# Kernel optimization log

Measured on AMD Instinct MI355X. Metric: run time of the kernel, lower is better.

Reference implementation:

```python
import jax, jax.numpy as jnp
import numpy as np

B, S, DIN, DOUT, A, T, H = 8, 1024, 1024, 1024, 4, 4, 8  # arity A, T cell types, hidden H


def setup_inputs() -> dict:
    key = jax.random.key(0)
    ks = jax.random.split(key, 6)
    x = jax.random.normal(ks[0], (B, S, DIN), jnp.float32)
    sc = 1.0 / np.sqrt(DIN).astype(np.float32)
    weight = jax.random.uniform(ks[1], (A * DOUT, DIN), jnp.float32, -sc, sc)
    bias = jax.random.uniform(ks[2], (A * DOUT,), jnp.float32, -sc, sc)
    # stacked per-cell-type MLP params: arity -> H -> 1 (tanh)
    cw1 = jax.random.normal(ks[3], (T, A, H), jnp.float32) / np.sqrt(A).astype(np.float32)
    cb1 = jnp.zeros((T, H), jnp.float32)
    cw2 = jax.random.normal(ks[4], (T, H), jnp.float32) / np.sqrt(H).astype(np.float32)
    cb2 = jnp.zeros((T,), jnp.float32)
    return {"x": x, "weight": weight, "bias": bias,
            "cw1": cw1, "cb1": cb1, "cw2": cw2, "cb2": cb2}


def reference(x, weight, bias, cw1, cb1, cw2, cb2):
    T_, A_, H_ = cw1.shape
    Dout = weight.shape[0] // A_
    G = Dout // T_  # neurons per cell type (cell_indices = contiguous blocks via np.repeat)
    # all_inputs = F.linear(input, weight, bias): (B, S, A*Dout)
    z = jnp.einsum('bsd,od->bso', x, weight) + bias
    # slice per-neuron arity chunks -> (B, S, T, G, A)
    z = z.reshape(z.shape[0], z.shape[1], T_, G, A_)
    # per-cell-type MLP applied to every neuron of that type (replaces Python loop)
    h = jnp.tanh(jnp.einsum('bstga,tah->bstgh', z, cw1) + cb1[:, None, :])
    o = jnp.einsum('bstgh,th->bstg', h, cw2) + cb2[:, None]
    # concat over neurons -> (B, S, Dout)
    return o.reshape(o.shape[0], o.shape[1], Dout)
```

## Files before the change

kernel.cpp:

```cpp
#include <hip/hip_runtime.h>


typedef __bf16 bf16x8 __attribute__((ext_vector_type(8)));
typedef float f32x4 __attribute__((ext_vector_type(4)));
typedef float f32x16 __attribute__((ext_vector_type(16)));

#define BM 256
#define BN 128
#define BK 64
#define KDIM 1024
#define A_ELEMS (BM * BK)
#define ZSTRIDE 132
#define XN8 (8192 * 1024 / 8)
#define WN8 (4096 * 1024 / 8)

__global__ __launch_bounds__(256) void cvt_bf16_kernel(
    const float* __restrict__ x, const float* __restrict__ w,
    __bf16* __restrict__ xb, __bf16* __restrict__ wb) {
    int i = blockIdx.x * 256 + threadIdx.x;
    const float* src;
    __bf16* dst;
    int j;
    if (i < XN8) { src = x; dst = xb; j = i; }
    else         { src = w; dst = wb; j = i - XN8; }
    const f32x4* p = (const f32x4*)src + 2 * (size_t)j;
    f32x4 a = p[0], b = p[1];
    bf16x8 o;
    o[0] = (__bf16)a[0]; o[1] = (__bf16)a[1]; o[2] = (__bf16)a[2]; o[3] = (__bf16)a[3];
    o[4] = (__bf16)b[0]; o[5] = (__bf16)b[1]; o[6] = (__bf16)b[2]; o[7] = (__bf16)b[3];
    ((bf16x8*)dst)[j] = o;
}

union __align__(16) SmemU {
    __bf16 stg[A_ELEMS + BN * BK];
    float  z[64 * ZSTRIDE];
};

__global__ __launch_bounds__(256, 2) void fused_gemm_mlp_kernel(
    const __bf16* __restrict__ Ag,
    const __bf16* __restrict__ Bg,
    const float* __restrict__ bias,
    const float* __restrict__ cw1,
    const float* __restrict__ cb1,
    const float* __restrict__ cw2,
    const float* __restrict__ cb2,
    float* __restrict__ out)
{
    __shared__ SmemU u;

    const int tid  = threadIdx.x;
    const int wave = tid >> 6;
    const int lane = tid & 63;
    const int wm = wave >> 1;
    const int wn = wave & 1;
    const int bn0 = blockIdx.x * BN;
    const int bm0 = blockIdx.y * BM;

    f32x16 acc[4][2] = {};

    const int srow  = lane >> 3;
    const int scol8 = (((lane & 7) ^ srow) * 8);

    const int lr5 = lane & 31;
    const int lk2 = lane >> 5;
    const int lx  = lane & 7;
    int a_base[4], b_base[4];
#pragma unroll
    for (int kh = 0; kh < 4; ++kh) {
        const int cx = ((kh * 2 + lk2) ^ lx) * 16;
        a_base[kh] = (wm * 128 + lr5) * (BK * 2) + cx;
        b_base[kh] = A_ELEMS * 2 + (wn * 64 + lr5) * (BK * 2) + cx;
    }
    const char* sb = (const char*)u.stg;

    for (int k0 = 0; k0 < KDIM; k0 += BK) {
#pragma unroll
        for (int c = 0; c < 8; ++c) {
            const int chunk = wave + c * 4;
            const __bf16* ga = Ag + (size_t)(bm0 + chunk * 8 + srow) * KDIM + k0 + scol8;
            __builtin_amdgcn_global_load_lds(
                (__attribute__((address_space(1))) void*)ga,
                (__attribute__((address_space(3))) void*)&u.stg[chunk * 8 * BK],
                16, 0, 0);
        }
#pragma unroll
        for (int c = 0; c < 4; ++c) {
            const int chunk = wave + c * 4;
            const __bf16* gb = Bg + (size_t)(bn0 + chunk * 8 + srow) * KDIM + k0 + scol8;
            __builtin_amdgcn_global_load_lds(
                (__attribute__((address_space(1))) void*)gb,
                (__attribute__((address_space(3))) void*)&u.stg[A_ELEMS + chunk * 8 * BK],
                16, 0, 0);
        }
        __syncthreads();

#pragma unroll
        for (int kh = 0; kh < 4; ++kh) {
            bf16x8 af[4], bfr[2];
#pragma unroll
            for (int mi = 0; mi < 4; ++mi)
                af[mi] = *(const bf16x8*)(sb + a_base[kh] + mi * 4096);
#pragma unroll
            for (int ni = 0; ni < 2; ++ni)
                bfr[ni] = *(const bf16x8*)(sb + b_base[kh] + ni * 4096);
#pragma unroll
            for (int mi = 0; mi < 4; ++mi)
#pragma unroll
                for (int ni = 0; ni < 2; ++ni)
                    acc[mi][ni] = __builtin_amdgcn_mfma_f32_32x32x16_bf16(
                        af[mi], bfr[ni], acc[mi][ni], 0, 0, 0);
        }
        __syncthreads();
    }

    const int t = bn0 >> 10;
    float w1[32], b1[8], w2[8];
#pragma unroll
    for (int i = 0; i < 32; ++i) w1[i] = cw1[t * 32 + i];
#pragma unroll
    for (int i = 0; i < 8; ++i) { b1[i] = cb1[t * 8 + i]; w2[i] = cw2[t * 8 + i]; }
    const float b2 = cb2[t];

    float bcol[2];
#pragma unroll
    for (int ni = 0; ni < 2; ++ni)
        bcol[ni] = bias[bn0 + wn * 64 + ni * 32 + lr5];

    const float L2E2 = 2.885390081777927f;

#pragma unroll
    for (int h = 0; h < 4; ++h) {
        if (wm == (h >> 1)) {
            const int mi0 = (h & 1) * 2;
#pragma unroll
            for (int dmi = 0; dmi < 2; ++dmi) {
                const int mi = mi0 + dmi;
#pragma unroll
                for (int ni = 0; ni < 2; ++ni) {
                    const int n = wn * 64 + ni * 32 + lr5;
#pragma unroll
                    for (int g = 0; g < 4; ++g) {
                        const int rb = dmi * 32 + g * 8 + lk2 * 4;
                        u.z[(rb + 0) * ZSTRIDE + n] = acc[mi][ni][g * 4 + 0] + bcol[ni];
                        u.z[(rb + 1) * ZSTRIDE + n] = acc[mi][ni][g * 4 + 1] + bcol[ni];
                        u.z[(rb + 2) * ZSTRIDE + n] = acc[mi][ni][g * 4 + 2] + bcol[ni];
                        u.z[(rb + 3) * ZSTRIDE + n] = acc[mi][ni][g * 4 + 3] + bcol[ni];
                    }
                }
            }
        }
        __syncthreads();

#pragma unroll
        for (int it = 0; it < 8; ++it) {
            const int i = tid + it * 256;
            const int q = i & 31;
            const int r = i >> 5;
            f32x4 z = *(const f32x4*)&u.z[r * ZSTRIDE + 4 * q];
            float o = 0.f;
#pragma unroll
            for (int hh = 0; hh < 8; ++hh) {
                float pre = z[0] * w1[0 * 8 + hh] + z[1] * w1[1 * 8 + hh]
                          + z[2] * w1[2 * 8 + hh] + z[3] * w1[3 * 8 + hh] + b1[hh];
                float e = __builtin_amdgcn_exp2f(pre * L2E2);
                float th = 1.0f - 2.0f * __builtin_amdgcn_rcpf(e + 1.0f);
                o += th * w2[hh];
            }
            o += b2;
            out[(size_t)(bm0 + h * 64 + r) * 1024 + (bn0 >> 2) + q] = o;
        }
        __syncthreads();
    }
}

extern "C" void kernel_launch(void* const* d_in, const int* in_sizes, int n_in,
                              void* d_out, int out_size, void* d_ws, size_t ws_size,
                              hipStream_t stream) {
    const float* x    = (const float*)d_in[0];
    const float* w    = (const float*)d_in[1];
    const float* bias = (const float*)d_in[2];
    const float* cw1  = (const float*)d_in[3];
    const float* cb1  = (const float*)d_in[4];
    const float* cw2  = (const float*)d_in[5];
    const float* cb2  = (const float*)d_in[6];
    float* out = (float*)d_out;

    __bf16* xb = (__bf16*)d_ws;
    __bf16* wb = xb + (size_t)8192 * 1024;

    cvt_bf16_kernel<<<(XN8 + WN8) / 256, 256, 0, stream>>>(x, w, xb, wb);

    dim3 grid(4096 / BN, 8192 / BM);
    fused_gemm_mlp_kernel<<<grid, 256, 0, stream>>>(xb, wb, bias, cw1, cb1, cw2, cb2, out);
}
```

Baseline: 192.0 us.

## Double-buffer 256x256 GEMM tiles with 8 waves and interleaved async staging

Grows the block tile to 256x256 with 512 threads (8 waves in a 2x4 grid) and double-buffers the A/B LDS tiles. Global-to-LDS loads for the next K step are issued in four phases interleaved with MFMA groups, using partial vmcnt waits, raw barriers and setprio around MFMA bursts. The aim is to hide global load latency behind compute and to raise arithmetic intensity per block. In exchange it needs 128KB of LDS per block, which likely limits occupancy to one block per CU, and the barrier and waitcnt ordering is fragile.

```diff
diff --git a/kernel.cpp b/kernel.cpp
--- a/kernel.cpp
+++ b/kernel.cpp
@@ -6,11 +6,13 @@
 typedef float f32x16 __attribute__((ext_vector_type(16)));
 
 #define BM 256
-#define BN 128
+#define BN 256
 #define BK 64
 #define KDIM 1024
-#define A_ELEMS (BM * BK)
-#define ZSTRIDE 132
+#define NT 16
+#define BUFB 65536
+#define BBASE 32768
+#define ZS 260
 #define XN8 (8192 * 1024 / 8)
 #define WN8 (4096 * 1024 / 8)
 
@@ -32,11 +34,14 @@
 }
 
 union __align__(16) SmemU {
-    __bf16 stg[A_ELEMS + BN * BK];
-    float  z[64 * ZSTRIDE];
+    unsigned char raw[2 * BUFB];
+    float z[64 * ZS];
 };
 
-__global__ __launch_bounds__(256, 2) void fused_gemm_mlp_kernel(
+#define FENCE() asm volatile("" ::: "memory")
+#define BARRIER() do { FENCE(); __builtin_amdgcn_s_barrier(); FENCE(); } while (0)
+
+__global__ __launch_bounds__(512, 2) void fused_gemm_mlp_kernel(
     const __bf16* __restrict__ Ag,
     const __bf16* __restrict__ Bg,
     const float* __restrict__ bias,
@@ -51,12 +56,10 @@
     const int tid  = threadIdx.x;
     const int wave = tid >> 6;
     const int lane = tid & 63;
-    const int wm = wave >> 1;
-    const int wn = wave & 1;
+    const int wm = wave >> 2;
+    const int wn = wave & 3;
     const int bn0 = blockIdx.x * BN;
     const int bm0 = blockIdx.y * BM;
-
-    f32x16 acc[4][2] = {};
 
     const int srow  = lane >> 3;
     const int scol8 = (((lane & 7) ^ srow) * 8);
@@ -64,62 +67,133 @@
     const int lr5 = lane & 31;
     const int lk2 = lane >> 5;
     const int lx  = lane & 7;
-    int a_base[4], b_base[4];
-#pragma unroll
-    for (int kh = 0; kh < 4; ++kh) {
-        const int cx = ((kh * 2 + lk2) ^ lx) * 16;
-        a_base[kh] = (wm * 128 + lr5) * (BK * 2) + cx;
-        b_base[kh] = A_ELEMS * 2 + (wn * 64 + lr5) * (BK * 2) + cx;
+    const int lg  = lr5 >> 3;
+    int aoff[4], boff[2], slot[4];
+#pragma unroll
+    for (int mi = 0; mi < 4; ++mi) aoff[mi] = (wm * 16 + mi * 4 + lg) * 1024 + lx * 128;
+#pragma unroll
+    for (int ni = 0; ni < 2; ++ni) boff[ni] = BBASE + (wn * 8 + ni * 4 + lg) * 1024 + lx * 128;
+#pragma unroll
+    for (int ks = 0; ks < 4; ++ks) slot[ks] = ((ks * 2 + lk2) ^ lx) * 16;
+
+    const char* sb = (const char*)u.raw;
+
+    auto stageA = [&](int t, int half) {
+        if (t >= NT) return;
+        const int dst = (t & 1) * BUFB + (half * 16 + wave * 2) * 1024;
+        const __bf16* g = Ag + (size_t)(bm0 + half * 128 + wave * 16 + srow) * KDIM
+                        + t * BK + scol8;
+        __builtin_amdgcn_global_load_lds(
+            (__attribute__((address_space(1))) void*)g,
+            (__attribute__((address_space(3))) void*)&u.raw[dst], 16, 0, 0);
+        __builtin_amdgcn_global_load_lds(
+            (__attribute__((address_space(1))) void*)(g + 8 * KDIM),
+            (__attribute__((address_space(3))) void*)&u.raw[dst + 1024], 16, 0, 0);
+    };
+    auto stageB = [&](int t, int half) {
+        if (t >= NT) return;
+        const int dst = (t & 1) * BUFB + BBASE + (half * 16 + wave * 2) * 1024;
+        const __bf16* g = Bg + (size_t)(bn0 + half * 128 + wave * 16 + srow) * KDIM
+                        + t * BK + scol8;
+        __builtin_amdgcn_global_load_lds(
+            (__attribute__((address_space(1))) void*)g,
+            (__attribute__((address_space(3))) void*)&u.raw[dst], 16, 0, 0);
+        __builtin_amdgcn_global_load_lds(
+            (__attribute__((address_space(1))) void*)(g + 8 * KDIM),
+            (__attribute__((address_space(3))) void*)&u.raw[dst + 1024], 16, 0, 0);
+    };
+
+    f32x16 acc[4][2] = {};
+    bf16x8 aA[8];
+    bf16x8 a1f[8];
+    bf16x8 bf0[4], bf1[4];
+
+    stageB(0, 0); stageB(0, 1); stageA(0, 0); stageA(0, 1); stageB(1, 0);
+    asm volatile("s_waitcnt vmcnt(2)" ::: "memory");
+    BARRIER();
+#pragma unroll
+    for (int mi = 0; mi < 2; ++mi)
+#pragma unroll
+        for (int ks = 0; ks < 4; ++ks)
+            aA[mi * 4 + ks] = *(const bf16x8*)(sb + aoff[mi] + slot[ks]);
+    stageB(1, 1);
+
+#pragma unroll 2
+    for (int T = 0; T < NT; ++T) {
+        const int buf  = (T & 1) * BUFB;
+        const int nbuf = buf ^ BUFB;
+
+        BARRIER();
+#pragma unroll
+        for (int ks = 0; ks < 4; ++ks)
+            bf0[ks] = *(const bf16x8*)(sb + buf + boff[0] + slot[ks]);
+        stageA(T + 1, 0);
+        __builtin_amdgcn_s_setprio(1);
+#pragma unroll
+        for (int mi = 0; mi < 2; ++mi)
+#pragma unroll
+            for (int ks = 0; ks < 4; ++ks)
+                acc[mi][0] = __builtin_amdgcn_mfma_f32_32x32x16_bf16(
+                    aA[mi * 4 + ks], bf0[ks], acc[mi][0], 0, 0, 0);
+        __builtin_amdgcn_s_setprio(0);
+
+        BARRIER();
+#pragma unroll
+        for (int ks = 0; ks < 4; ++ks)
+            bf1[ks] = *(const bf16x8*)(sb + buf + boff[1] + slot[ks]);
+        stageA(T + 1, 1);
+        __builtin_amdgcn_s_setprio(1);
+#pragma unroll
+        for (int mi = 0; mi < 2; ++mi)
+#pragma unroll
+            for (int ks = 0; ks < 4; ++ks)
+                acc[mi][1] = __builtin_amdgcn_mfma_f32_32x32x16_bf16(
+                    aA[mi * 4 + ks], bf1[ks], acc[mi][1], 0, 0, 0);
+        __builtin_amdgcn_s_setprio(0);
+
+        BARRIER();
+#pragma unroll
+        for (int mi = 0; mi < 2; ++mi)
+#pragma unroll
+            for (int ks = 0; ks < 4; ++ks)
+                a1f[mi * 4 + ks] = *(const bf16x8*)(sb + buf + aoff[2 + mi] + slot[ks]);
+        stageB(T + 2, 0);
+        __builtin_amdgcn_s_setprio(1);
+#pragma unroll
+        for (int mi = 0; mi < 2; ++mi)
+#pragma unroll
+            for (int ks = 0; ks < 4; ++ks)
+                acc[2 + mi][0] = __builtin_amdgcn_mfma_f32_32x32x16_bf16(
+                    a1f[mi * 4 + ks], bf0[ks], acc[2 + mi][0], 0, 0, 0);
+        __builtin_amdgcn_s_setprio(0);
+        asm volatile("s_waitcnt vmcnt(2)" ::: "memory");
+
+        BARRIER();
+        if (T + 1 < NT) {
+#pragma unroll
+            for (int mi = 0; mi < 2; ++mi)
+#pragma unroll
+                for (int ks = 0; ks < 4; ++ks)
+                    aA[mi * 4 + ks] = *(const bf16x8*)(sb + nbuf + aoff[mi] + slot[ks]);
+        }
+        stageB(T + 2, 1);
+        __builtin_amdgcn_s_setprio(1);
+#pragma unroll
+        for (int mi = 0; mi < 2; ++mi)
+#pragma unroll
+            for (int ks = 0; ks < 4; ++ks)
+                acc[2 + mi][1] = __builtin_amdgcn_mfma_f32_32x32x16_bf16(
+                    a1f[mi * 4 + ks], bf1[ks], acc[2 + mi][1], 0, 0, 0);
+        __builtin_amdgcn_s_setprio(0);
     }
-    const char* sb = (const char*)u.stg;
-
-    for (int k0 = 0; k0 < KDIM; k0 += BK) {
-#pragma unroll
-        for (int c = 0; c < 8; ++c) {
-            const int chunk = wave + c * 4;
-            const __bf16* ga = Ag + (size_t)(bm0 + chunk * 8 + srow) * KDIM + k0 + scol8;
-            __builtin_amdgcn_global_load_lds(
-                (__attribute__((address_space(1))) void*)ga,
-                (__attribute__((address_space(3))) void*)&u.stg[chunk * 8 * BK],
-                16, 0, 0);
-        }
-#pragma unroll
-        for (int c = 0; c < 4; ++c) {
-            const int chunk = wave + c * 4;
-            const __bf16* gb = Bg + (size_t)(bn0 + chunk * 8 + srow) * KDIM + k0 + scol8;
-            __builtin_amdgcn_global_load_lds(
-                (__attribute__((address_space(1))) void*)gb,
-                (__attribute__((address_space(3))) void*)&u.stg[A_ELEMS + chunk * 8 * BK],
-                16, 0, 0);
-        }
-        __syncthreads();
-
-#pragma unroll
-        for (int kh = 0; kh < 4; ++kh) {
-            bf16x8 af[4], bfr[2];
-#pragma unroll
-            for (int mi = 0; mi < 4; ++mi)
-                af[mi] = *(const bf16x8*)(sb + a_base[kh] + mi * 4096);
-#pragma unroll
-            for (int ni = 0; ni < 2; ++ni)
-                bfr[ni] = *(const bf16x8*)(sb + b_base[kh] + ni * 4096);
-#pragma unroll
-            for (int mi = 0; mi < 4; ++mi)
-#pragma unroll
-                for (int ni = 0; ni < 2; ++ni)
-                    acc[mi][ni] = __builtin_amdgcn_mfma_f32_32x32x16_bf16(
-                        af[mi], bfr[ni], acc[mi][ni], 0, 0, 0);
-        }
-        __syncthreads();
-    }
-
-    const int t = bn0 >> 10;
+
+    const int tct = bn0 >> 10;
     float w1[32], b1[8], w2[8];
 #pragma unroll
-    for (int i = 0; i < 32; ++i) w1[i] = cw1[t * 32 + i];
-#pragma unroll
-    for (int i = 0; i < 8; ++i) { b1[i] = cb1[t * 8 + i]; w2[i] = cw2[t * 8 + i]; }
-    const float b2 = cb2[t];
+    for (int i = 0; i < 32; ++i) w1[i] = cw1[tct * 32 + i];
+#pragma unroll
+    for (int i = 0; i < 8; ++i) { b1[i] = cb1[tct * 8 + i]; w2[i] = cw2[tct * 8 + i]; }
+    const float b2 = cb2[tct];
 
     float bcol[2];
 #pragma unroll
@@ -127,6 +201,9 @@
         bcol[ni] = bias[bn0 + wn * 64 + ni * 32 + lr5];
 
     const float L2E2 = 2.885390081777927f;
+
+    asm volatile("s_waitcnt vmcnt(0)" ::: "memory");
+    __syncthreads();
 
 #pragma unroll
     for (int h = 0; h < 4; ++h) {
@@ -134,17 +211,16 @@
             const int mi0 = (h & 1) * 2;
 #pragma unroll
             for (int dmi = 0; dmi < 2; ++dmi) {
-                const int mi = mi0 + dmi;
 #pragma unroll
                 for (int ni = 0; ni < 2; ++ni) {
                     const int n = wn * 64 + ni * 32 + lr5;
 #pragma unroll
                     for (int g = 0; g < 4; ++g) {
                         const int rb = dmi * 32 + g * 8 + lk2 * 4;
-                        u.z[(rb + 0) * ZSTRIDE + n] = acc[mi][ni][g * 4 + 0] + bcol[ni];
-                        u.z[(rb + 1) * ZSTRIDE + n] = acc[mi][ni][g * 4 + 1] + bcol[ni];
-                        u.z[(rb + 2) * ZSTRIDE + n] = acc[mi][ni][g * 4 + 2] + bcol[ni];
-                        u.z[(rb + 3) * ZSTRIDE + n] = acc[mi][ni][g * 4 + 3] + bcol[ni];
+                        u.z[(rb + 0) * ZS + n] = acc[mi0 + dmi][ni][g * 4 + 0] + bcol[ni];
+                        u.z[(rb + 1) * ZS + n] = acc[mi0 + dmi][ni][g * 4 + 1] + bcol[ni];
+                        u.z[(rb + 2) * ZS + n] = acc[mi0 + dmi][ni][g * 4 + 2] + bcol[ni];
+                        u.z[(rb + 3) * ZS + n] = acc[mi0 + dmi][ni][g * 4 + 3] + bcol[ni];
                     }
                 }
             }
@@ -153,15 +229,15 @@
 
 #pragma unroll
         for (int it = 0; it < 8; ++it) {
-            const int i = tid + it * 256;
-            const int q = i & 31;
-            const int r = i >> 5;
-            f32x4 z = *(const f32x4*)&u.z[r * ZSTRIDE + 4 * q];
+            const int i = tid + it * 512;
+            const int q = i & 63;
+            const int r = i >> 6;
+            f32x4 z4 = *(const f32x4*)&u.z[r * ZS + 4 * q];
             float o = 0.f;
 #pragma unroll
             for (int hh = 0; hh < 8; ++hh) {
-                float pre = z[0] * w1[0 * 8 + hh] + z[1] * w1[1 * 8 + hh]
-                          + z[2] * w1[2 * 8 + hh] + z[3] * w1[3 * 8 + hh] + b1[hh];
+                float pre = z4[0] * w1[0 * 8 + hh] + z4[1] * w1[1 * 8 + hh]
+                          + z4[2] * w1[2 * 8 + hh] + z4[3] * w1[3 * 8 + hh] + b1[hh];
                 float e = __builtin_amdgcn_exp2f(pre * L2E2);
                 float th = 1.0f - 2.0f * __builtin_amdgcn_rcpf(e + 1.0f);
                 o += th * w2[hh];
@@ -191,5 +267,5 @@
     cvt_bf16_kernel<<<(XN8 + WN8) / 256, 256, 0, stream>>>(x, w, xb, wb);
 
     dim3 grid(4096 / BN, 8192 / BM);
-    fused_gemm_mlp_kernel<<<grid, 256, 0, stream>>>(xb, wb, bias, cw1, cb1, cw2, cb2, out);
+    fused_gemm_mlp_kernel<<<grid, 512, 0, stream>>>(xb, wb, bias, cw1, cb1, cw2, cb2, out);
 }
```

Measured after the change: 195.8 us. Within noise of the previous version (+2.0%).

## Double-buffer LDS staging with BK=32 to overlap global loads with MFMA

Applied to the files above, without the earlier changes.

Halves the K tile to 32 and allocates two LDS stage buffers of the same total size, so the global_load_lds for tile t+1 is issued before the MFMAs on tile t run. It also introduces a new swizzled layout that packs two rows per 128-byte line. The aim is to hide global-to-LDS latency behind compute. The cost is twice as many K iterations and barriers, and LDS occupancy stays the same. The diff does not show the loop-end sync, and if that sync is missing there may be a race on buffer reuse.

```diff
diff --git a/kernel.cpp b/kernel.cpp
--- a/kernel.cpp
+++ b/kernel.cpp
@@ -7,9 +7,11 @@
 
 #define BM 256
 #define BN 128
-#define BK 64
+#define BK 32
 #define KDIM 1024
-#define A_ELEMS (BM * BK)
+#define NT 32
+#define ABUF 16384
+#define BUFB 24576
 #define ZSTRIDE 132
 #define XN8 (8192 * 1024 / 8)
 #define WN8 (4096 * 1024 / 8)
@@ -32,8 +34,8 @@
 }
 
 union __align__(16) SmemU {
-    __bf16 stg[A_ELEMS + BN * BK];
-    float  z[64 * ZSTRIDE];
+    unsigned char raw[2 * BUFB];
+    float z[64 * ZSTRIDE];
 };
 
 __global__ __launch_bounds__(256, 2) void fused_gemm_mlp_kernel(
@@ -58,51 +60,63 @@
 
     f32x16 acc[4][2] = {};
 
-    const int srow  = lane >> 3;
-    const int scol8 = (((lane & 7) ^ srow) * 8);
+    const int qloc = lane >> 3;
+    const int slog = (lane & 7) ^ qloc;
+    const int arow = 2 * qloc + (slog >> 2);
+    const int acol = (slog & 3) * 8;
 
     const int lr5 = lane & 31;
     const int lk2 = lane >> 5;
-    const int lx  = lane & 7;
-    int a_base[4], b_base[4];
-#pragma unroll
-    for (int kh = 0; kh < 4; ++kh) {
-        const int cx = ((kh * 2 + lk2) ^ lx) * 16;
-        a_base[kh] = (wm * 128 + lr5) * (BK * 2) + cx;
-        b_base[kh] = A_ELEMS * 2 + (wn * 64 + lr5) * (BK * 2) + cx;
+    const int lrh = lr5 >> 1;
+    const int lp  = lr5 & 1;
+    int a_addr[2], b_addr[2];
+#pragma unroll
+    for (int kh = 0; kh < 2; ++kh) {
+        const int slot = (((lp * 4) + (kh * 2 + lk2)) ^ (lrh & 7)) * 16;
+        a_addr[kh] = wm * 8192 + lrh * 128 + slot;
+        b_addr[kh] = ABUF + wn * 4096 + lrh * 128 + slot;
     }
-    const char* sb = (const char*)u.stg;
-
-    for (int k0 = 0; k0 < KDIM; k0 += BK) {
-#pragma unroll
-        for (int c = 0; c < 8; ++c) {
-            const int chunk = wave + c * 4;
-            const __bf16* ga = Ag + (size_t)(bm0 + chunk * 8 + srow) * KDIM + k0 + scol8;
+    const char* sb = (const char*)u.raw;
+
+    auto stage = [&](int t) {
+        const int bb = (t & 1) * BUFB;
+        const int k0 = t * BK;
+#pragma unroll
+        for (int c = 0; c < 4; ++c) {
+            const int ch = wave + c * 4;
+            const __bf16* g = Ag + (size_t)(bm0 + ch * 16 + arow) * KDIM + k0 + acol;
             __builtin_amdgcn_global_load_lds(
-                (__attribute__((address_space(1))) void*)ga,
-                (__attribute__((address_space(3))) void*)&u.stg[chunk * 8 * BK],
+                (__attribute__((address_space(1))) void*)g,
+                (__attribute__((address_space(3))) void*)&u.raw[bb + ch * 1024],
                 16, 0, 0);
         }
 #pragma unroll
-        for (int c = 0; c < 4; ++c) {
-            const int chunk = wave + c * 4;
-            const __bf16* gb = Bg + (size_t)(bn0 + chunk * 8 + srow) * KDIM + k0 + scol8;
+        for (int c = 0; c < 2; ++c) {
+            const int ch = wave + c * 4;
+            const __bf16* g = Bg + (size_t)(bn0 + ch * 16 + arow) * KDIM + k0 + acol;
             __builtin_amdgcn_global_load_lds(
-                (__attribute__((address_space(1))) void*)gb,
-                (__attribute__((address_space(3))) void*)&u.stg[A_ELEMS + chunk * 8 * BK],
+                (__attribute__((address_space(1))) void*)g,
+                (__attribute__((address_space(3))) void*)&u.raw[bb + ABUF + ch * 1024],
                 16, 0, 0);
         }
-        __syncthreads();
-
-#pragma unroll
-        for (int kh = 0; kh < 4; ++kh) {
+    };
+
+    stage(0);
+    __syncthreads();
+
+    for (int t = 0; t < NT; ++t) {
+        if (t + 1 < NT) stage(t + 1);
+
+        const int cb = (t & 1) * BUFB;
+#pragma unroll
+        for (int kh = 0; kh < 2; ++kh) {
             bf16x8 af[4], bfr[2];
 #pragma unroll
             for (int mi = 0; mi < 4; ++mi)
-                af[mi] = *(const bf16x8*)(sb + a_base[kh] + mi * 4096);
+                af[mi] = *(const bf16x8*)(sb + cb + a_addr[kh] + mi * 2048);
 #pragma unroll
             for (int ni = 0; ni < 2; ++ni)
-                bfr[ni] = *(const bf16x8*)(sb + b_base[kh] + ni * 4096);
+                bfr[ni] = *(const bf16x8*)(sb + cb + b_addr[kh] + ni * 2048);
 #pragma unroll
             for (int mi = 0; mi < 4; ++mi)
 #pragma unroll
```

Measured after the change: 192.0 us. Within noise of the previous version (+0.0%).
